# Kernel tuning notes

Measured on AMD Instinct MI355X. Metric: run time of the kernel, lower is better.

Reference implementation:

```python
import jax, jax.numpy as jnp
import numpy as np

NUM_CLASSES = 101
BATCH = 262144
LAMBDA = 1000.0


def setup_inputs() -> dict:
    key = jax.random.key(0)
    k1, k2 = jax.random.split(key)
    outputs = jax.random.normal(k1, (BATCH, NUM_CLASSES), dtype=jnp.float32)
    targets = jax.random.randint(k2, (BATCH,), 0, NUM_CLASSES, dtype=jnp.int64)
    return {"outputs": outputs, "targets": targets}


def reference(outputs, targets):
    B, C = outputs.shape
    targets = targets.reshape(-1)
    tf = targets.astype(outputs.dtype)

    probs = jax.nn.softmax(outputs, axis=1)                      # [B, C]
    labels = jnp.arange(C, dtype=outputs.dtype)                  # [C]
    pred_values = jnp.sum(probs * labels[None, :], axis=1)       # [B]
    centered = labels[None, :] - pred_values[:, None]            # [B, C]
    variance = jnp.sum(probs * centered * centered, axis=1)      # [B]
    variance = jnp.clip(variance, 1e-6, None)
    est_err = (pred_values - tf) ** 2
    concentrated_loss = jnp.mean(0.5 * jnp.log(variance) + est_err / (2.0 * variance))

    # Unimodal ordinal penalty, vectorized over the original double loop:
    # sign_j = -1 if j < target else +1; penalty = relu(-(p_j - p_{j+1}) * sign_j)
    j = jnp.arange(C - 1)                                        # [C-1]
    sign = jnp.where(j[None, :] < targets[:, None], -1.0, 1.0).astype(outputs.dtype)
    prob_diff = probs[:, :-1] - probs[:, 1:]                     # [B, C-1]
    penalty = jax.nn.relu(-prob_diff * sign)
    unimodal_loss = jnp.sum(penalty) / B
    weighted_unimodal_loss = LAMBDA * unimodal_loss

    total_loss = concentrated_loss + weighted_unimodal_loss
    return (total_loss, concentrated_loss, weighted_unimodal_loss)
```

## Files before the change

### kernel.cpp

```cpp
#include <hip/hip_runtime.h>


#define NC 101
#define LAMBDA_W 1000.0

template <int CTRL>
__device__ __forceinline__ float dpp_mov(float v) {
    return __int_as_float(__builtin_amdgcn_update_dpp(
        0, __float_as_int(v), CTRL, 0xf, 0xf, true));
}

__device__ __forceinline__ float team_sum16(float v) {
    v += dpp_mov<0x111>(v);
    v += dpp_mov<0x112>(v);
    v += dpp_mov<0x114>(v);
    v += dpp_mov<0x118>(v);
    return v;
}

__global__ __launch_bounds__(256)
void ucl_stream_kernel(const float* __restrict__ x,
                       const int* __restrict__ tgt,
                       float2* __restrict__ partial,
                       int ngroups)
{
    const int tid  = threadIdx.x;
    const int lane = tid & 63;
    const int s    = lane & 15;
    const int gwave  = blockIdx.x * 4 + (tid >> 6);
    const int nwaves = gridDim.x * 4;

    const float fs = (float)s;
    float conc = 0.f, pens = 0.f;

    for (int g = gwave; g < ngroups; g += nwaves) {
        const int row = g * 4 + (lane >> 4);
        const float* __restrict__ xr = x + (size_t)row * NC;
        const int t = tgt[row];

        float e[7];
#pragma unroll
        for (int k = 0; k < 7; ++k) {
            const int j = s + 16 * k;
            e[k] = (j < NC) ? xr[j] : 0.f;
        }
#pragma unroll
        for (int k = 0; k < 7; ++k) {
            const int j = s + 16 * k;
            float ee = __expf(e[k]);
            e[k] = (j < NC) ? ee : 0.f;
        }

        float S = 0.f, W = 0.f, Q = 0.f;
#pragma unroll
        for (int k = 0; k < 7; ++k) {
            const float fj = fs + (float)(16 * k);
            S += e[k];
            W = fmaf(e[k], fj, W);
            Q = fmaf(e[k], fj * fj, Q);
        }

        float pen = 0.f;
#pragma unroll
        for (int k = 0; k < 7; ++k) {
            float n1 = dpp_mov<0x101>(e[k]);
            float nx = (k < 6) ? dpp_mov<0x11F>(e[k + 1])
                               : 0.f;
            float en = (s == 15) ? nx : n1;
            float d  = e[k] - en;
            pen += fmaxf(d, 0.f);
            const int j = s + 16 * k;
            pen -= (j == t) ? e[k] : 0.f;
        }

        S   = team_sum16(S);
        W   = team_sum16(W);
        Q   = team_sum16(Q);
        pen = team_sum16(pen);

        if (s == 15) {
            float pred = W / S;
            float var  = fmaxf(fmaf(-pred, pred, Q / S), 1e-6f);
            float err  = pred - (float)t;
            conc += 0.5f * __logf(var) + err * err / (2.0f * var);
            pens += pen / S;
        }
    }

    conc += __shfl_down(conc, 16);
    pens += __shfl_down(pens, 16);
    conc += __shfl_down(conc, 32);
    pens += __shfl_down(pens, 32);

    __shared__ float red[8];
    if (lane == 15) {
        red[(tid >> 6) * 2 + 0] = conc;
        red[(tid >> 6) * 2 + 1] = pens;
    }
    __syncthreads();
    if (tid == 0)
        partial[blockIdx.x] = make_float2(red[0] + red[2] + red[4] + red[6],
                                          red[1] + red[3] + red[5] + red[7]);
}

__global__ __launch_bounds__(256)
void ucl_finalize(const float2* __restrict__ partial,
                  float* __restrict__ out,
                  int nblocks, double invB)
{
    const int tid = threadIdx.x;
    double c = 0.0, p = 0.0;
    for (int i = tid; i < nblocks; i += 256) {
        float2 v = partial[i];
        c += (double)v.x;
        p += (double)v.y;
    }
#pragma unroll
    for (int off = 32; off > 0; off >>= 1) {
        c += __shfl_down(c, off);
        p += __shfl_down(p, off);
    }
    __shared__ double sm[8];
    if ((tid & 63) == 0) { sm[(tid >> 6) * 2] = c; sm[(tid >> 6) * 2 + 1] = p; }
    __syncthreads();
    if (tid == 0) {
        double C = (sm[0] + sm[2] + sm[4] + sm[6]) * invB;
        double P = (sm[1] + sm[3] + sm[5] + sm[7]) * invB * LAMBDA_W;
        out[0] = (float)(C + P);
        out[1] = (float)C;
        out[2] = (float)P;
    }
}

extern "C" void kernel_launch(void* const* d_in, const int* in_sizes, int n_in,
                              void* d_out, int out_size, void* d_ws, size_t ws_size,
                              hipStream_t stream)
{
    const float* x   = (const float*)d_in[0];
    const int*   tgt = (const int*)d_in[1];
    float* out = (float*)d_out;
    float2* partial = (float2*)d_ws;

    const int B = in_sizes[1];
    const int ngroups = B / 4;
    const int blocks = 1024;

    hipLaunchKernelGGL(ucl_stream_kernel, dim3(blocks), dim3(256), 0, stream,
                       x, tgt, partial, ngroups);
    hipLaunchKernelGGL(ucl_finalize, dim3(1), dim3(256), 0, stream,
                       partial, out, blocks, 1.0 / (double)B);
}
```

Before: 154.9 us.

## Double-buffer row groups into LDS via async global_load_lds prefetch

Each wave now streams its 4-row group (1616 bytes plus targets) into a per-wave double-buffered LDS window with global_load_lds, prefetching the next group while computing the current one, and synchronizes with explicit vmcnt waits. This is meant to hide global load latency and replace scattered per-lane strided loads with aligned 16-byte wide loads. It adds LDS traffic and hand-written waitcnt assumptions, and the final group falls back to direct global loads to avoid reading past the end of the buffer.

```diff
diff --git a/kernel.cpp b/kernel.cpp
--- a/kernel.cpp
+++ b/kernel.cpp
@@ -3,6 +3,16 @@
 
 #define NC 101
 #define LAMBDA_W 1000.0
+#define GRPB 1616u
+#define WINB 2048u
+#define WINF 512
+
+typedef const void __attribute__((address_space(1)))* as1_cptr;
+typedef void __attribute__((address_space(3)))* as3_ptr;
+
+__device__ __forceinline__ void gload_lds16(const void* g, void* l) {
+    __builtin_amdgcn_global_load_lds((as1_cptr)g, (as3_ptr)l, 16, 0, 0);
+}
 
 template <int CTRL>
 __device__ __forceinline__ float dpp_mov(float v) {
@@ -27,28 +37,67 @@
     const int tid  = threadIdx.x;
     const int lane = tid & 63;
     const int s    = lane & 15;
-    const int gwave  = blockIdx.x * 4 + (tid >> 6);
+    const int r    = lane >> 4;
+    const int wid  = tid >> 6;
+    const int gwave  = blockIdx.x * 4 + wid;
     const int nwaves = gridDim.x * 4;
+
+    __shared__ float smem[4][2][528];
+    const uint32_t total_b = (uint32_t)ngroups * GRPB;
+    const char* xb = (const char*)x;
 
     const float fs = (float)s;
     float conc = 0.f, pens = 0.f;
 
+    auto prefetch = [&](int gn, int nb) -> int {
+        uint32_t start = (uint32_t)gn * GRPB;
+        uint32_t base  = start & ~255u;
+        if (base > total_b - WINB) base = total_b - WINB;
+        const char* src = xb + base + ((uint32_t)lane << 4);
+        float* dst = &smem[wid][nb][0];
+        gload_lds16(src, dst);
+        gload_lds16(src + 1024, (char*)dst + 1024);
+        if (lane == 0)
+            gload_lds16((const char*)tgt + (uint32_t)gn * 16u,
+                        (char*)dst + 2048);
+        return (int)((start - base) >> 2);
+    };
+
+    int cur  = 0;
+    int dcur = prefetch(gwave, 0);
+
     for (int g = gwave; g < ngroups; g += nwaves) {
-        const int row = g * 4 + (lane >> 4);
-        const float* __restrict__ xr = x + (size_t)row * NC;
-        const int t = tgt[row];
+        const int gnext = g + nwaves;
+        int dnext = 0;
+        if (gnext < ngroups) {
+            dnext = prefetch(gnext, cur ^ 1);
+            asm volatile("s_waitcnt vmcnt(3)" ::: "memory");
+        } else {
+            asm volatile("s_waitcnt vmcnt(0)" ::: "memory");
+        }
+
+        const float* buf = &smem[wid][cur][0];
+        const int t = ((const int*)(buf + WINF))[r];
 
         float e[7];
-#pragma unroll
-        for (int k = 0; k < 7; ++k) {
-            const int j = s + 16 * k;
-            e[k] = (j < NC) ? xr[j] : 0.f;
-        }
-#pragma unroll
-        for (int k = 0; k < 7; ++k) {
-            const int j = s + 16 * k;
-            float ee = __expf(e[k]);
-            e[k] = (j < NC) ? ee : 0.f;
+        if (g != ngroups - 1) {
+            const int boff = dcur + 101 * r + s;
+#pragma unroll
+            for (int k = 0; k < 7; ++k) {
+                const int j = s + 16 * k;
+                float v  = buf[boff + 16 * k];
+                float ee = __expf(v);
+                e[k] = (j < NC) ? ee : 0.f;
+            }
+        } else {
+            const float* xr = x + (size_t)(g * 4 + r) * NC;
+#pragma unroll
+            for (int k = 0; k < 7; ++k) {
+                const int j = s + 16 * k;
+                float v  = (j < NC) ? xr[j] : 0.f;
+                float ee = __expf(v);
+                e[k] = (j < NC) ? ee : 0.f;
+            }
         }
 
         float S = 0.f, W = 0.f, Q = 0.f;
@@ -85,6 +134,9 @@
             conc += 0.5f * __logf(var) + err * err / (2.0f * var);
             pens += pen / S;
         }
+
+        cur ^= 1;
+        dcur = dnext;
     }
 
     conc += __shfl_down(conc, 16);
@@ -94,8 +146,8 @@
 
     __shared__ float red[8];
     if (lane == 15) {
-        red[(tid >> 6) * 2 + 0] = conc;
-        red[(tid >> 6) * 2 + 1] = pens;
+        red[wid * 2 + 0] = conc;
+        red[wid * 2 + 1] = pens;
     }
     __syncthreads();
     if (tid == 0)
```

New measurement: 156.6 us. No clear change (+1.1%).

## Stage row groups through LDS with float4 loads and register prefetch

Applied to the files above, without the earlier changes.

Each wave now loads its contiguous 4-row group (404 floats) with coalesced 16-byte vector loads into registers, writes it to a per-wave LDS slot, and reads the per-lane elements back from LDS. The next group's data is prefetched into registers one iteration ahead so global latency overlaps the current group's compute. This replaces strided scalar global loads with wide vectorized ones. In exchange it adds LDS traffic and more register use, and it has no barrier between the LDS write and the read that follows it, which relies on wave-level lockstep execution.

```diff
diff --git a/kernel.cpp b/kernel.cpp
--- a/kernel.cpp
+++ b/kernel.cpp
@@ -2,7 +2,10 @@
 
 
 #define NC 101
+#define GRPF 404
 #define LAMBDA_W 1000.0
+
+typedef float f4 __attribute__((ext_vector_type(4)));
 
 template <int CTRL>
 __device__ __forceinline__ float dpp_mov(float v) {
@@ -27,27 +30,45 @@
     const int tid  = threadIdx.x;
     const int lane = tid & 63;
     const int s    = lane & 15;
-    const int gwave  = blockIdx.x * 4 + (tid >> 6);
+    const int r    = lane >> 4;
+    const int wid  = tid >> 6;
+    const int gwave  = blockIdx.x * 4 + wid;
     const int nwaves = gridDim.x * 4;
+
+    __shared__ float slot[4][GRPF + 12];
 
     const float fs = (float)s;
     float conc = 0.f, pens = 0.f;
 
+    f4 a = {0.f, 0.f, 0.f, 0.f}, b = {0.f, 0.f, 0.f, 0.f};
+    if (gwave < ngroups) {
+        const f4* gp = (const f4*)(x + (size_t)gwave * GRPF);
+        a = gp[lane];
+        if (lane < 37) b = gp[64 + lane];
+    }
+
     for (int g = gwave; g < ngroups; g += nwaves) {
-        const int row = g * 4 + (lane >> 4);
-        const float* __restrict__ xr = x + (size_t)row * NC;
-        const int t = tgt[row];
+        const int gn = g + nwaves;
+        f4 an = {0.f, 0.f, 0.f, 0.f}, bn = {0.f, 0.f, 0.f, 0.f};
+        if (gn < ngroups) {
+            const f4* gp = (const f4*)(x + (size_t)gn * GRPF);
+            an = gp[lane];
+            if (lane < 37) bn = gp[64 + lane];
+        }
 
+        const int t = tgt[g * 4 + r];
+
+        f4* sp = (f4*)&slot[wid][0];
+        sp[lane] = a;
+        if (lane < 37) sp[64 + lane] = b;
+
+        const float* buf = &slot[wid][101 * r];
         float e[7];
 #pragma unroll
         for (int k = 0; k < 7; ++k) {
             const int j = s + 16 * k;
-            e[k] = (j < NC) ? xr[j] : 0.f;
-        }
-#pragma unroll
-        for (int k = 0; k < 7; ++k) {
-            const int j = s + 16 * k;
-            float ee = __expf(e[k]);
+            float v  = (j < NC) ? buf[j] : 0.f;
+            float ee = __expf(v);
             e[k] = (j < NC) ? ee : 0.f;
         }
 
@@ -85,6 +106,8 @@
             conc += 0.5f * __logf(var) + err * err / (2.0f * var);
             pens += pen / S;
         }
+
+        a = an; b = bn;
     }
 
     conc += __shfl_down(conc, 16);
@@ -94,8 +117,8 @@
 
     __shared__ float red[8];
     if (lane == 15) {
-        red[(tid >> 6) * 2 + 0] = conc;
-        red[(tid >> 6) * 2 + 1] = pens;
+        red[wid * 2 + 0] = conc;
+        red[wid * 2 + 1] = pens;
     }
     __syncthreads();
     if (tid == 0)
```

Measured after the change: 156.7 us. Within noise of the previous version (+1.2%).
